# Kernel optimization log

Measured on AMD Instinct MI355X. Metric: run time of the kernel, lower is better.

## Reference

```python
import jax, jax.numpy as jnp
import numpy as np

N_NODES, N_EDGES, IN_F = 20000, 320000, 64
H1, H2 = 2, 2          # attn heads per GATv2 layer
D1, D2 = 128, 128      # gnn_size per layer
NM = [128, 128]        # nodemlp hidden sizes
EM = [512, 256]        # edgemlp hidden sizes
OUT_F = 1
NEG_SLOPE = 0.2


def _lin_init(key, fan_in, fan_out):
    kw, kb = jax.random.split(key)
    s = 1.0 / np.sqrt(fan_in)
    return (jax.random.uniform(kw, (fan_in, fan_out), jnp.float32, -s, s),
            jax.random.uniform(kb, (fan_out,), jnp.float32, -s, s))


def setup_inputs() -> dict:
    key = jax.random.key(0)
    ks = jax.random.split(key, 16)
    x = jax.random.normal(ks[0], (N_NODES, IN_F), jnp.float32)
    src = jax.random.randint(ks[1], (N_EDGES,), 0, N_NODES, jnp.int32)
    dst = jax.random.randint(ks[2], (N_EDGES,), 0, N_NODES, jnp.int32)
    # NodeMLP
    nw0, nb0 = _lin_init(ks[3], IN_F, NM[0])
    nw1, nb1 = _lin_init(ks[4], NM[0], NM[1])
    # GATv2 layer 1 (in=IN_F -> H1*D1)
    g1ws, g1bs = _lin_init(ks[5], IN_F, H1 * D1)
    g1wd, g1bd = _lin_init(ks[6], IN_F, H1 * D1)
    g1a = jax.random.normal(ks[7], (H1, D1), jnp.float32) * (1.0 / np.sqrt(D1))
    # GATv2 layer 2 (in=H1*D1 -> H2*D2)
    g2ws, g2bs = _lin_init(ks[8], H1 * D1, H2 * D2)
    g2wd, g2bd = _lin_init(ks[9], H1 * D1, H2 * D2)
    g2a = jax.random.normal(ks[10], (H2, D2), jnp.float32) * (1.0 / np.sqrt(D2))
    # EdgeMLP: in = 2*(NM[-1] + H2*D2) = 768
    e_in = 2 * (NM[-1] + H2 * D2)
    ew0, eb0 = _lin_init(ks[11], e_in, EM[0])
    ew1, eb1 = _lin_init(ks[12], EM[0], EM[1])
    ew2, eb2 = _lin_init(ks[13], EM[1], OUT_F)
    return dict(x=x, src=src, dst=dst,
                nw0=nw0, nb0=nb0, nw1=nw1, nb1=nb1,
                g1ws=g1ws, g1bs=g1bs, g1wd=g1wd, g1bd=g1bd, g1a=g1a,
                g2ws=g2ws, g2bs=g2bs, g2wd=g2wd, g2bd=g2bd, g2a=g2a,
                ew0=ew0, eb0=eb0, ew1=ew1, eb1=eb1, ew2=ew2, eb2=eb2)


def _segment_softmax(logits, dst, n):
    # logits: (E, H); softmax over edges sharing the same dst node
    m = jax.ops.segment_max(logits, dst, num_segments=n)
    e = jnp.exp(logits - m[dst])
    s = jax.ops.segment_sum(e, dst, num_segments=n)
    return e / s[dst]


def _gatv2(h, src, dst, ws, bs, wd, bd, attn, heads, dim, n):
    fs = (h @ ws + bs).reshape(n, heads, dim)   # fc_src
    fd = (h @ wd + bd).reshape(n, heads, dim)   # fc_dst
    e = jax.nn.leaky_relu(fs[src] + fd[dst], NEG_SLOPE)      # (E,H,D)
    logits = jnp.einsum('ehd,hd->eh', e, attn)               # (E,H)
    a = _segment_softmax(logits, dst, n)                      # (E,H)
    out = jax.ops.segment_sum(a[..., None] * fs[src], dst, num_segments=n)
    return jax.nn.relu(out).reshape(n, heads * dim)           # flatten heads


def reference(x, src, dst,
              nw0, nb0, nw1, nb1,
              g1ws, g1bs, g1wd, g1bd, g1a,
              g2ws, g2bs, g2wd, g2bd, g2a,
              ew0, eb0, ew1, eb1, ew2, eb2):
    n = x.shape[0]
    # NodeMLP (dropout=0 -> identity)
    h1 = jax.nn.relu(x @ nw0 + nb0)
    h1 = jax.nn.relu(h1 @ nw1 + nb1)
    # GCN: two GATv2Conv layers with relu activation, heads flattened
    h2 = _gatv2(x, src, dst, g1ws, g1bs, g1wd, g1bd, g1a, H1, D1, n)
    h2 = _gatv2(h2, src, dst, g2ws, g2bs, g2wd, g2bd, g2a, H2, D2, n)
    # EdgeMLP: gather src/dst, concat, MLP (relu before every layer but first)
    h = jnp.concatenate([h1[src], h1[dst], h2[src], h2[dst]], axis=1)  # (E,768)
    h = h @ ew0 + eb0
    h = jax.nn.relu(h) @ ew1 + eb1
    h = jax.nn.relu(h) @ ew2 + eb2
    return h  # (E, 1) edge scores
```

## Files before the change

### kernel.cpp

```cpp
#include <hip/hip_runtime.h>
#include <hip/hip_bf16.h>

constexpr int N_NODES = 20000;
constexpr int N_EDGES = 320000;

typedef _Float16 half8 __attribute__((ext_vector_type(8)));
typedef _Float16 half4 __attribute__((ext_vector_type(4)));
typedef float    f32x16 __attribute__((ext_vector_type(16)));

__device__ __forceinline__ float lrelu(float x) { return x > 0.f ? x : 0.2f * x; }

__global__ void hist_kernel(const int* __restrict__ dst, int* __restrict__ counts) {
    int e = blockIdx.x * 256 + threadIdx.x;
    if (e < N_EDGES) atomicAdd(&counts[dst[e]], 1);
}

__global__ void scan_all_kernel(const int* __restrict__ counts,
                                int* __restrict__ row_off, int* __restrict__ cursor) {
    __shared__ int ps[1024];
    const int t = threadIdx.x;
    const int base = t * 20;
    int loc[20];
    int sum = 0;
#pragma unroll
    for (int i = 0; i < 20; ++i) {
        const int idx = base + i;
        const int v = (idx < N_NODES) ? counts[idx] : 0;
        loc[i] = sum;
        sum += v;
    }
    ps[t] = sum;
    __syncthreads();
    for (int off = 1; off < 1024; off <<= 1) {
        const int v = (t >= off) ? ps[t - off] : 0;
        __syncthreads();
        ps[t] += v;
        __syncthreads();
    }
    const int ex = ps[t] - sum;
#pragma unroll
    for (int i = 0; i < 20; ++i) {
        const int idx = base + i;
        if (idx < N_NODES) {
            row_off[idx] = ex + loc[i];
            cursor[idx]  = ex + loc[i];
        }
    }
    if (t == 0) row_off[N_NODES] = N_EDGES;
}

__global__ void scatter_kernel(const int* __restrict__ src, const int* __restrict__ dst,
                               int* __restrict__ cursor, int* __restrict__ eidx,
                               int* __restrict__ srcs) {
    int e = blockIdx.x * 256 + threadIdx.x;
    if (e < N_EDGES) {
        int p = atomicAdd(&cursor[dst[e]], 1);
        eidx[p] = e;
        srcs[p] = src[e];
    }
}

template <int K, int M>
__device__ __forceinline__ void pack_one(int idx, const float* __restrict__ W,
                                         int r1, int k1, int r2, int joff, int ldw,
                                         _Float16* __restrict__ H,
                                         _Float16* __restrict__ L) {
    const int l  = idx & 63;
    const int t  = (idx >> 6) % (M / 32);
    const int s  = (idx >> 6) / (M / 32);
    const int j  = joff + t * 32 + (l & 31);
    const int kb = s * 16 + (l >> 5) * 8;
    half8 vh, vl;
#pragma unroll
    for (int i = 0; i < 8; ++i) {
        const int k    = kb + i;
        const int rrow = (k < k1) ? (r1 + k) : (r2 + (k - k1));
        const float w  = W[(size_t)rrow * ldw + j];
        const _Float16 h = (_Float16)w;
        vh[i] = h;
        vl[i] = (_Float16)(w - (float)h);
    }
    reinterpret_cast<half8*>(H)[idx] = vh;
    reinterpret_cast<half8*>(L)[idx] = vl;
}

constexpr int OFF_W1  = 0;
constexpr int OFF_G2S = 16384;
constexpr int OFF_G2D = 24576;
constexpr int OFF_SW0 = 32768;
constexpr int OFF_SW1 = 45056;
constexpr int OFF_DW0 = 57344;
constexpr int OFF_DW1 = 69632;
constexpr int OFF_N1  = 81920;
constexpr int OFF_X   = 83968;
constexpr int PACK_TOT = 89088;

struct PackIn {
    const float *ew1, *g1ws, *g1wd, *g2ws, *g2wd, *ew0, *nw0, *nw1;
    _Float16 *H, *L;
};

__global__ void prepack_all_kernel(PackIn a) {
    const int idx = blockIdx.x * 256 + threadIdx.x;
    if (idx >= PACK_TOT) return;
    _Float16* H = a.H;
    _Float16* L = a.L;
    if (idx < OFF_G2S)
        pack_one<512, 256>(idx - OFF_W1, a.ew1, 0, 512, 0, 0, 256,
                           H + OFF_W1 * 8, L + OFF_W1 * 8);
    else if (idx < OFF_G2D)
        pack_one<256, 256>(idx - OFF_G2S, a.g2ws, 0, 256, 0, 0, 256,
                           H + OFF_G2S * 8, L + OFF_G2S * 8);
    else if (idx < OFF_SW0)
        pack_one<256, 256>(idx - OFF_G2D, a.g2wd, 0, 256, 0, 0, 256,
                           H + OFF_G2D * 8, L + OFF_G2D * 8);
    else if (idx < OFF_SW1)
        pack_one<384, 256>(idx - OFF_SW0, a.ew0, 0, 128, 256, 0, 512,
                           H + OFF_SW0 * 8, L + OFF_SW0 * 8);
    else if (idx < OFF_DW0)
        pack_one<384, 256>(idx - OFF_SW1, a.ew0, 0, 128, 256, 256, 512,
                           H + OFF_SW1 * 8, L + OFF_SW1 * 8);
    else if (idx < OFF_DW1)
        pack_one<384, 256>(idx - OFF_DW0, a.ew0, 128, 128, 512, 0, 512,
                           H + OFF_DW0 * 8, L + OFF_DW0 * 8);
    else if (idx < OFF_N1)
        pack_one<384, 256>(idx - OFF_DW1, a.ew0, 128, 128, 512, 256, 512,
                           H + OFF_DW1 * 8, L + OFF_DW1 * 8);
    else if (idx < OFF_X)
        pack_one<128, 128>(idx - OFF_N1, a.nw1, 0, 128, 0, 0, 128,
                           H + OFF_N1 * 8, L + OFF_N1 * 8);
    else {
        const int xi  = idx - OFF_X;
        const int seg = xi >> 10, r = xi & 1023;
        const int sb  = OFF_X + seg * 1024;
        if (seg == 0)
            pack_one<64, 128>(r, a.nw0, 0, 64, 0, 0, 128, H + sb * 8, L + sb * 8);
        else if (seg <= 2)
            pack_one<64, 128>(r, a.g1ws, 0, 64, 0, (seg - 1) * 128, 256,
                              H + sb * 8, L + sb * 8);
        else
            pack_one<64, 128>(r, a.g1wd, 0, 64, 0, (seg - 3) * 128, 256,
                              H + sb * 8, L + sb * 8);
    }
}

struct LinOut { float* y[6]; const float* b[6]; _Float16* yh[6]; int ldy[6]; int relu[6]; };

template <int K, int TJ, int WR, int K1, int LD1, int LD2, int MINW, int SEG>
__global__ __launch_bounds__(256, MINW) void mfma_linear2_kernel(
    const float* __restrict__ X1, const float* __restrict__ X2,
    const _Float16* __restrict__ BHp, const _Float16* __restrict__ BLp,
    LinOut lo, int N) {
    constexpr int WC    = 4 / WR;
    constexpr int TILES = WC * TJ;
    const int jb  = blockIdx.y;
    const int tid = threadIdx.x;
    const int wv  = tid >> 6, l = tid & 63;
    const int rg  = (WR == 1) ? 0 : ((WR == 4) ? wv : (wv & 1));
    const int cg  = (WR == 1) ? wv : ((WR == 4) ? 0 : (wv >> 1));
    const int m   = l & 31, h = l >> 5;
    const int row = blockIdx.x * (32 * WR) + rg * 32 + m;
    const int ar  = (row < N) ? row : (N - 1);
    const float* __restrict__ xr1 = X1 + (size_t)ar * LD1;
    const float* __restrict__ xr2 = X2 + (size_t)ar * LD2;
    const half8* __restrict__ BH = reinterpret_cast<const half8*>(BHp) + (size_t)jb * SEG;
    const half8* __restrict__ BL = reinterpret_cast<const half8*>(BLp) + (size_t)jb * SEG;
    const float* __restrict__ bp = lo.b[jb];
    float* __restrict__ Y = lo.y[jb];
    _Float16* __restrict__ Yh = lo.yh[jb];
    const int ldy = lo.ldy[jb];
    const int rel = lo.relu[jb];

    f32x16 acc[TJ];
#pragma unroll
    for (int jt = 0; jt < TJ; ++jt) {
        const float bv = bp ? bp[cg * TJ * 32 + jt * 32 + m] : 0.f;
#pragma unroll
        for (int r = 0; r < 16; ++r) acc[jt][r] = bv;
    }

    const int kf = h * 8;
    const float* pf = (kf < K1) ? (xr1 + kf) : (xr2 + (kf - K1));
    float4 xa = *reinterpret_cast<const float4*>(pf);
    float4 xb = *reinterpret_cast<const float4*>(pf + 4);

    for (int s = 0; s < K / 16; ++s) {
        const float xs[8] = {xa.x, xa.y, xa.z, xa.w, xb.x, xb.y, xb.z, xb.w};
        if (s + 1 < K / 16) {
            const int kn = (s + 1) * 16 + h * 8;
            const float* pn = (kn < K1) ? (xr1 + kn) : (xr2 + (kn - K1));
            xa = *reinterpret_cast<const float4*>(pn);
            xb = *reinterpret_cast<const float4*>(pn + 4);
        }
        half8 ah, al;
#pragma unroll
        for (int i = 0; i < 8; ++i) {
            const _Float16 hi = (_Float16)xs[i];
            ah[i] = hi;
            al[i] = (_Float16)(xs[i] - (float)hi);
        }
#pragma unroll
        for (int jt = 0; jt < TJ; ++jt) {
            const int fi = (s * TILES + cg * TJ + jt) * 64 + l;
            const half8 bh = BH[fi];
            const half8 bl = BL[fi];
            acc[jt] = __builtin_amdgcn_mfma_f32_32x32x16_f16(ah, bh, acc[jt], 0, 0, 0);
            acc[jt] = __builtin_amdgcn_mfma_f32_32x32x16_f16(al, bh, acc[jt], 0, 0, 0);
            acc[jt] = __builtin_amdgcn_mfma_f32_32x32x16_f16(ah, bl, acc[jt], 0, 0, 0);
        }
    }

    const int rbase = blockIdx.x * (32 * WR) + rg * 32;
#pragma unroll
    for (int jt = 0; jt < TJ; ++jt) {
        const int j = cg * TJ * 32 + jt * 32 + m;
#pragma unroll
        for (int r = 0; r < 16; ++r) {
            const int orow = rbase + (r & 3) + 8 * (r >> 2) + 4 * h;
            if (orow < N) {
                float v = acc[jt][r];
                if (rel) v = fmaxf(v, 0.f);
                if (Y)  Y[(size_t)orow * ldy + j] = v;
                if (Yh) Yh[(size_t)orow * ldy + j] = (_Float16)v;
            }
        }
    }
}

__global__ void gat_fused_kernel(const _Float16* __restrict__ fsh,
                                 const float* __restrict__ fd,
                                 const float* __restrict__ attn,
                                 const int* __restrict__ row_off,
                                 const int* __restrict__ srcs,
                                 float* __restrict__ outp) {
    const int wv = threadIdx.x >> 6, l = threadIdx.x & 63;
    const int n = blockIdx.x * 4 + wv;
    if (n >= N_NODES) return;
    const int base = (l >> 5) * 128 + (l & 31) * 4;
    const float4 fdv = *reinterpret_cast<const float4*>(&fd[n * 256 + base]);
    const float4 av  = *reinterpret_cast<const float4*>(&attn[base]);
    const int s0 = row_off[n], s1 = row_off[n + 1];

    auto LD = [&](int k) {
        return *reinterpret_cast<const half4*>(&fsh[(size_t)srcs[k] * 256 + base]);
    };
    auto LOGIT = [&](const float4& v) {
        float p = lrelu(v.x + fdv.x) * av.x;
        p = fmaf(lrelu(v.y + fdv.y), av.y, p);
        p = fmaf(lrelu(v.z + fdv.z), av.z, p);
        p = fmaf(lrelu(v.w + fdv.w), av.w, p);
        return p;
    };

    float m = -INFINITY, lsum = 0.f;
    float4 acc = {0.f, 0.f, 0.f, 0.f};
    half4 c0 = {0, 0, 0, 0}, c1 = {0, 0, 0, 0}, n0 = {0, 0, 0, 0}, n1 = {0, 0, 0, 0};
    int i = s0;
    if (i     < s1) c0 = LD(i);
    if (i + 1 < s1) c1 = LD(i + 1);
    if (i + 2 < s1) n0 = LD(i + 2);
    if (i + 3 < s1) n1 = LD(i + 3);
    for (; i + 1 < s1; i += 2) {
        const float4 v0 = {(float)c0.x, (float)c0.y, (float)c0.z, (float)c0.w};
        const float4 v1 = {(float)c1.x, (float)c1.y, (float)c1.z, (float)c1.w};
        c0 = n0; c1 = n1;
        if (i + 4 < s1) n0 = LD(i + 4);
        if (i + 5 < s1) n1 = LD(i + 5);
        float p0 = LOGIT(v0);
        float p1 = LOGIT(v1);
#pragma unroll
        for (int off = 1; off < 32; off <<= 1) {
            p0 += __shfl_xor(p0, off);
            p1 += __shfl_xor(p1, off);
        }
        const float mn = fmaxf(m, fmaxf(p0, p1));
        const float alpha = __expf(m - mn);
        const float w0 = __expf(p0 - mn), w1 = __expf(p1 - mn);
        lsum = fmaf(lsum, alpha, w0 + w1);
        acc.x = fmaf(w1, v1.x, fmaf(w0, v0.x, acc.x * alpha));
        acc.y = fmaf(w1, v1.y, fmaf(w0, v0.y, acc.y * alpha));
        acc.z = fmaf(w1, v1.z, fmaf(w0, v0.z, acc.z * alpha));
        acc.w = fmaf(w1, v1.w, fmaf(w0, v0.w, acc.w * alpha));
        m = mn;
    }
    if (i < s1) {
        const float4 v0 = {(float)c0.x, (float)c0.y, (float)c0.z, (float)c0.w};
        float p0 = LOGIT(v0);
#pragma unroll
        for (int off = 1; off < 32; off <<= 1) p0 += __shfl_xor(p0, off);
        const float mn = fmaxf(m, p0);
        const float alpha = __expf(m - mn);
        const float w0 = __expf(p0 - mn);
        lsum = fmaf(lsum, alpha, w0);
        acc.x = fmaf(w0, v0.x, acc.x * alpha);
        acc.y = fmaf(w0, v0.y, acc.y * alpha);
        acc.z = fmaf(w0, v0.z, acc.z * alpha);
        acc.w = fmaf(w0, v0.w, acc.w * alpha);
    }
    const float inv = (s1 > s0) ? 1.f / lsum : 0.f;
    float4 o;
    o.x = fmaxf(acc.x * inv, 0.f);
    o.y = fmaxf(acc.y * inv, 0.f);
    o.z = fmaxf(acc.z * inv, 0.f);
    o.w = fmaxf(acc.w * inv, 0.f);
    *reinterpret_cast<float4*>(&outp[n * 256 + base]) = o;
}

__global__ __launch_bounds__(256, 2) void edge_mlp8_kernel(
    const _Float16* __restrict__ S, const _Float16* __restrict__ Dn,
    const int* __restrict__ srcs, const int* __restrict__ eidx,
    const int* __restrict__ dstf,
    const _Float16* __restrict__ WpH,
    const float* __restrict__ b1, const float* __restrict__ w2,
    const float* __restrict__ b2, float* __restrict__ out) {
    const int tid = threadIdx.x;
    const int wv  = tid >> 6, l = tid & 63;
    const int m   = l & 31, h = l >> 5;
    const int e0  = blockIdx.x * 128;
    const int slot = e0 + wv * 32 + m;
    const _Float16* __restrict__ Srow = S  + (size_t)srcs[slot] * 512;
    const _Float16* __restrict__ Drow = Dn + (size_t)dstf[eidx[slot]] * 512;
    const half8* __restrict__ Bp = reinterpret_cast<const half8*>(WpH);

    f32x16 acc[8];
#pragma unroll
    for (int jt = 0; jt < 8; ++jt) {
        const float bv = b1[jt * 32 + m];
#pragma unroll
        for (int r = 0; r < 16; ++r) acc[jt][r] = bv;
    }

    half8 bA[8], bB[8];
#pragma unroll
    for (int jt = 0; jt < 8; ++jt) bA[jt] = Bp[jt * 64 + l];
    half8 sv = *reinterpret_cast<const half8*>(Srow + h * 8);
    half8 dv = *reinterpret_cast<const half8*>(Drow + h * 8);

    for (int s = 0; s < 32; s += 2) {
        half8 xh;
#pragma unroll
        for (int i = 0; i < 8; ++i) {
            const _Float16 t = sv[i] + dv[i];
            xh[i] = t > (_Float16)0.f ? t : (_Float16)0.f;
        }
        {
            const int ko = (s + 1) * 16 + h * 8;
            sv = *reinterpret_cast<const half8*>(Srow + ko);
            dv = *reinterpret_cast<const half8*>(Drow + ko);
        }
#pragma unroll
        for (int jt = 0; jt < 8; ++jt)
            bB[jt] = Bp[(size_t)((s + 1) * 8 + jt) * 64 + l];
#pragma unroll
        for (int jt = 0; jt < 8; ++jt)
            acc[jt] = __builtin_amdgcn_mfma_f32_32x32x16_f16(xh, bA[jt], acc[jt], 0, 0, 0);

        half8 xh2;
#pragma unroll
        for (int i = 0; i < 8; ++i) {
            const _Float16 t = sv[i] + dv[i];
            xh2[i] = t > (_Float16)0.f ? t : (_Float16)0.f;
        }
        if (s + 2 < 32) {
            const int ko = (s + 2) * 16 + h * 8;
            sv = *reinterpret_cast<const half8*>(Srow + ko);
            dv = *reinterpret_cast<const half8*>(Drow + ko);
#pragma unroll
            for (int jt = 0; jt < 8; ++jt)
                bA[jt] = Bp[(size_t)((s + 2) * 8 + jt) * 64 + l];
        }
#pragma unroll
        for (int jt = 0; jt < 8; ++jt)
            acc[jt] = __builtin_amdgcn_mfma_f32_32x32x16_f16(xh2, bB[jt], acc[jt], 0, 0, 0);
    }

    float part[16];
#pragma unroll
    for (int r = 0; r < 16; ++r) part[r] = 0.f;
#pragma unroll
    for (int jt = 0; jt < 8; ++jt) {
        const float w2v = w2[jt * 32 + m];
#pragma unroll
        for (int r = 0; r < 16; ++r)
            part[r] = fmaf(fmaxf(acc[jt][r], 0.f), w2v, part[r]);
    }
#pragma unroll
    for (int off = 1; off < 32; off <<= 1)
#pragma unroll
        for (int r = 0; r < 16; ++r) part[r] += __shfl_xor(part[r], off);
    if (m == 0) {
        const float b2v = b2[0];
#pragma unroll
        for (int r = 0; r < 16; ++r) {
            const int row = (r & 3) + 8 * (r >> 2) + 4 * h;
            out[eidx[e0 + wv * 32 + row]] = part[r] + b2v;
        }
    }
}

extern "C" void kernel_launch(void* const* d_in, const int* in_sizes, int n_in,
                              void* d_out, int out_size, void* d_ws, size_t ws_size,
                              hipStream_t stream) {
    (void)in_sizes; (void)n_in; (void)out_size; (void)ws_size;
    const float* x    = (const float*)d_in[0];
    const int*   src  = (const int*)d_in[1];
    const int*   dst  = (const int*)d_in[2];
    const float* nw0  = (const float*)d_in[3];
    const float* nb0  = (const float*)d_in[4];
    const float* nw1  = (const float*)d_in[5];
    const float* nb1  = (const float*)d_in[6];
    const float* g1ws = (const float*)d_in[7];
    const float* g1bs = (const float*)d_in[8];
    const float* g1wd = (const float*)d_in[9];
    const float* g1bd = (const float*)d_in[10];
    const float* g1a  = (const float*)d_in[11];
    const float* g2ws = (const float*)d_in[12];
    const float* g2bs = (const float*)d_in[13];
    const float* g2wd = (const float*)d_in[14];
    const float* g2bd = (const float*)d_in[15];
    const float* g2a  = (const float*)d_in[16];
    const float* ew0  = (const float*)d_in[17];
    const float* eb0  = (const float*)d_in[18];
    const float* ew1  = (const float*)d_in[19];
    const float* eb1  = (const float*)d_in[20];
    const float* ew2  = (const float*)d_in[21];
    const float* eb2  = (const float*)d_in[22];
    float* out = (float*)d_out;

    float* wsF = (float*)d_ws;
    float* h1  = wsF;
    float* g2o = wsF + 2560000;
    float* fsb = wsF + 7680000;
    float* fdb = wsF + 12800000;
    float* g1o = wsF + 17920000;
    _Float16* Sh = (_Float16*)(wsF + 7680000);
    _Float16* Dh = (_Float16*)(wsF + 12800000);
    _Float16* fsh = (_Float16*)(wsF + 23040000);
    int* wsI     = (int*)(wsF + 28160000);
    int* row_off = wsI;
    int* cursor  = wsI + 20016;
    int* eidx    = wsI + 40032;
    int* srcs    = wsI + 360032;
    _Float16* pkH = (_Float16*)((char*)d_ws + 115361280);
    _Float16* pkL = pkH + (size_t)PACK_TOT * 8;

    hipMemsetAsync(cursor, 0, N_NODES * sizeof(int), stream);
    hist_kernel<<<1250, 256, 0, stream>>>(dst, cursor);
    scan_all_kernel<<<1, 1024, 0, stream>>>(cursor, row_off, cursor);
    scatter_kernel<<<1250, 256, 0, stream>>>(src, dst, cursor, eidx, srcs);

    PackIn pin{ew1, g1ws, g1wd, g2ws, g2wd, ew0, nw0, nw1, pkH, pkL};
    prepack_all_kernel<<<(PACK_TOT + 255) / 256, 256, 0, stream>>>(pin);

    {   LinOut lo{};
        lo.y[0] = fsb;        lo.b[0] = nb0;        lo.ldy[0] = 128; lo.relu[0] = 1;
        lo.yh[1] = fsh;       lo.b[1] = g1bs;       lo.ldy[1] = 256;
        lo.yh[2] = fsh + 128; lo.b[2] = g1bs + 128; lo.ldy[2] = 256;
        lo.y[3] = fdb;        lo.b[3] = g1bd;       lo.ldy[3] = 256;
        lo.y[4] = fdb + 128;  lo.b[4] = g1bd + 128; lo.ldy[4] = 256;
        mfma_linear2_kernel<64, 1, 1, 64, 64, 64, 4, 1024>
            <<<dim3(625, 5), 256, 0, stream>>>(x, x, pkH + OFF_X * 8, pkL + OFF_X * 8,
                                               lo, N_NODES); }

    {   LinOut lo{};
        lo.y[0] = h1; lo.b[0] = nb1; lo.ldy[0] = 128; lo.relu[0] = 1;
        mfma_linear2_kernel<128, 1, 1, 128, 128, 128, 4, 0>
            <<<dim3(625, 1), 256, 0, stream>>>(fsb, fsb, pkH + OFF_N1 * 8, pkL + OFF_N1 * 8,
                                               lo, N_NODES); }

    gat_fused_kernel<<<5000, 256, 0, stream>>>(fsh, fdb, g1a, row_off, srcs, g1o);

    {   LinOut lo{};
        lo.yh[0] = fsh; lo.b[0] = g2bs; lo.ldy[0] = 256;
        lo.y[1] = fdb;  lo.b[1] = g2bd; lo.ldy[1] = 256;
        mfma_linear2_kernel<256, 8, 4, 256, 256, 256, 2, 8192>
            <<<dim3(157, 2), 256, 0, stream>>>(g1o, g1o, pkH + OFF_G2S * 8, pkL + OFF_G2S * 8,
                                               lo, N_NODES); }
    gat_fused_kernel<<<5000, 256, 0, stream>>>(fsh, fdb, g2a, row_off, srcs, g2o);

    {   LinOut lo{};
        lo.yh[0] = Sh;       lo.ldy[0] = 512;
        lo.yh[1] = Sh + 256; lo.ldy[1] = 512;
        lo.yh[2] = Dh;       lo.b[2] = eb0;       lo.ldy[2] = 512;
        lo.yh[3] = Dh + 256; lo.b[3] = eb0 + 256; lo.ldy[3] = 512;
        mfma_linear2_kernel<384, 8, 4, 128, 128, 256, 2, 12288>
            <<<dim3(157, 4), 256, 0, stream>>>(h1, g2o, pkH + OFF_SW0 * 8, pkL + OFF_SW0 * 8,
                                               lo, N_NODES); }

    edge_mlp8_kernel<<<N_EDGES / 128, 256, 0, stream>>>(Sh, Dh, srcs, eidx, dst,
                                                        pkH + OFF_W1 * 8,
                                                        eb1, ew2, eb2, out);
}
```

Before: 571.3 us.

## Stage edge-MLP weights in shared memory and drop softmax max tracking

The edge MLP kernel now loads each weight slice once per block and double-buffers it in LDS, with a block barrier every k-step. Previously every wave fetched the full weight slice from global memory into registers. This trades redundant global/L2 traffic and register pressure for 32 __syncthreads and LDS reads. The GAT aggregation also drops the online-softmax running max and rescaling, exponentiating raw logits directly. That removes per-edge exp and multiply work but risks overflow if logits are large.

Result: faster. 536.1 us (-6.2%).

```diff
diff --git a/kernel.cpp b/kernel.cpp
--- a/kernel.cpp
+++ b/kernel.cpp
@@ -252,7 +252,7 @@
         return p;
     };
 
-    float m = -INFINITY, lsum = 0.f;
+    float lsum = 0.f;
     float4 acc = {0.f, 0.f, 0.f, 0.f};
     half4 c0 = {0, 0, 0, 0}, c1 = {0, 0, 0, 0}, n0 = {0, 0, 0, 0}, n1 = {0, 0, 0, 0};
     int i = s0;
@@ -273,29 +273,24 @@
             p0 += __shfl_xor(p0, off);
             p1 += __shfl_xor(p1, off);
         }
-        const float mn = fmaxf(m, fmaxf(p0, p1));
-        const float alpha = __expf(m - mn);
-        const float w0 = __expf(p0 - mn), w1 = __expf(p1 - mn);
-        lsum = fmaf(lsum, alpha, w0 + w1);
-        acc.x = fmaf(w1, v1.x, fmaf(w0, v0.x, acc.x * alpha));
-        acc.y = fmaf(w1, v1.y, fmaf(w0, v0.y, acc.y * alpha));
-        acc.z = fmaf(w1, v1.z, fmaf(w0, v0.z, acc.z * alpha));
-        acc.w = fmaf(w1, v1.w, fmaf(w0, v0.w, acc.w * alpha));
-        m = mn;
+        const float w0 = __expf(p0), w1 = __expf(p1);
+        lsum += w0 + w1;
+        acc.x = fmaf(w1, v1.x, fmaf(w0, v0.x, acc.x));
+        acc.y = fmaf(w1, v1.y, fmaf(w0, v0.y, acc.y));
+        acc.z = fmaf(w1, v1.z, fmaf(w0, v0.z, acc.z));
+        acc.w = fmaf(w1, v1.w, fmaf(w0, v0.w, acc.w));
     }
     if (i < s1) {
         const float4 v0 = {(float)c0.x, (float)c0.y, (float)c0.z, (float)c0.w};
         float p0 = LOGIT(v0);
 #pragma unroll
         for (int off = 1; off < 32; off <<= 1) p0 += __shfl_xor(p0, off);
-        const float mn = fmaxf(m, p0);
-        const float alpha = __expf(m - mn);
-        const float w0 = __expf(p0 - mn);
-        lsum = fmaf(lsum, alpha, w0);
-        acc.x = fmaf(w0, v0.x, acc.x * alpha);
-        acc.y = fmaf(w0, v0.y, acc.y * alpha);
-        acc.z = fmaf(w0, v0.z, acc.z * alpha);
-        acc.w = fmaf(w0, v0.w, acc.w * alpha);
+        const float w0 = __expf(p0);
+        lsum += w0;
+        acc.x = fmaf(w0, v0.x, acc.x);
+        acc.y = fmaf(w0, v0.y, acc.y);
+        acc.z = fmaf(w0, v0.z, acc.z);
+        acc.w = fmaf(w0, v0.w, acc.w);
     }
     const float inv = (s1 > s0) ? 1.f / lsum : 0.f;
     float4 o;
@@ -306,13 +301,14 @@
     *reinterpret_cast<float4*>(&outp[n * 256 + base]) = o;
 }
 
-__global__ __launch_bounds__(256, 2) void edge_mlp8_kernel(
+__global__ __launch_bounds__(256, 2) void edge_mlp7_kernel(
     const _Float16* __restrict__ S, const _Float16* __restrict__ Dn,
     const int* __restrict__ srcs, const int* __restrict__ eidx,
     const int* __restrict__ dstf,
     const _Float16* __restrict__ WpH,
     const float* __restrict__ b1, const float* __restrict__ w2,
     const float* __restrict__ b2, float* __restrict__ out) {
+    __shared__ __align__(16) _Float16 Bs[2][8][512];
     const int tid = threadIdx.x;
     const int wv  = tid >> 6, l = tid & 63;
     const int m   = l & 31, h = l >> 5;
@@ -320,7 +316,6 @@
     const int slot = e0 + wv * 32 + m;
     const _Float16* __restrict__ Srow = S  + (size_t)srcs[slot] * 512;
     const _Float16* __restrict__ Drow = Dn + (size_t)dstf[eidx[slot]] * 512;
-    const half8* __restrict__ Bp = reinterpret_cast<const half8*>(WpH);
 
     f32x16 acc[8];
 #pragma unroll
@@ -330,48 +325,51 @@
         for (int r = 0; r < 16; ++r) acc[jt][r] = bv;
     }
 
-    half8 bA[8], bB[8];
-#pragma unroll
-    for (int jt = 0; jt < 8; ++jt) bA[jt] = Bp[jt * 64 + l];
+#pragma unroll
+    for (int c = 0; c < 2; ++c) {
+        const int jt = wv * 2 + c;
+        *reinterpret_cast<float4*>(&Bs[0][jt][l * 8]) =
+            *reinterpret_cast<const float4*>(WpH + ((size_t)jt * 64 + l) * 8);
+    }
     half8 sv = *reinterpret_cast<const half8*>(Srow + h * 8);
     half8 dv = *reinterpret_cast<const half8*>(Drow + h * 8);
-
-    for (int s = 0; s < 32; s += 2) {
+    __syncthreads();
+
+    for (int s = 0; s < 32; ++s) {
+        const int buf = s & 1;
+        float4 bst[2];
+        if (s < 31) {
+#pragma unroll
+            for (int c = 0; c < 2; ++c) {
+                const int jt = wv * 2 + c;
+                bst[c] = *reinterpret_cast<const float4*>(
+                    WpH + ((size_t)((s + 1) * 8 + jt) * 64 + l) * 8);
+            }
+        }
         half8 xh;
 #pragma unroll
         for (int i = 0; i < 8; ++i) {
             const _Float16 t = sv[i] + dv[i];
             xh[i] = t > (_Float16)0.f ? t : (_Float16)0.f;
         }
-        {
+        if (s < 31) {
             const int ko = (s + 1) * 16 + h * 8;
             sv = *reinterpret_cast<const half8*>(Srow + ko);
             dv = *reinterpret_cast<const half8*>(Drow + ko);
         }
 #pragma unroll
-        for (int jt = 0; jt < 8; ++jt)
-            bB[jt] = Bp[(size_t)((s + 1) * 8 + jt) * 64 + l];
-#pragma unroll
-        for (int jt = 0; jt < 8; ++jt)
-            acc[jt] = __builtin_amdgcn_mfma_f32_32x32x16_f16(xh, bA[jt], acc[jt], 0, 0, 0);
-
-        half8 xh2;
-#pragma unroll
-        for (int i = 0; i < 8; ++i) {
-            const _Float16 t = sv[i] + dv[i];
-            xh2[i] = t > (_Float16)0.f ? t : (_Float16)0.f;
-        }
-        if (s + 2 < 32) {
-            const int ko = (s + 2) * 16 + h * 8;
-            sv = *reinterpret_cast<const half8*>(Srow + ko);
-            dv = *reinterpret_cast<const half8*>(Drow + ko);
-#pragma unroll
-            for (int jt = 0; jt < 8; ++jt)
-                bA[jt] = Bp[(size_t)((s + 2) * 8 + jt) * 64 + l];
-        }
-#pragma unroll
-        for (int jt = 0; jt < 8; ++jt)
-            acc[jt] = __builtin_amdgcn_mfma_f32_32x32x16_f16(xh2, bB[jt], acc[jt], 0, 0, 0);
+        for (int jt = 0; jt < 8; ++jt) {
+            const half8 bh = *reinterpret_cast<const half8*>(&Bs[buf][jt][l * 8]);
+            acc[jt] = __builtin_amdgcn_mfma_f32_32x32x16_f16(xh, bh, acc[jt], 0, 0, 0);
+        }
+        if (s < 31) {
+#pragma unroll
+            for (int c = 0; c < 2; ++c) {
+                const int jt = wv * 2 + c;
+                *reinterpret_cast<float4*>(&Bs[buf ^ 1][jt][l * 8]) = bst[c];
+            }
+        }
+        __syncthreads();
     }
 
     float part[16];
@@ -487,7 +485,7 @@
             <<<dim3(157, 4), 256, 0, stream>>>(h1, g2o, pkH + OFF_SW0 * 8, pkL + OFF_SW0 * 8,
                                                lo, N_NODES); }
 
-    edge_mlp8_kernel<<<N_EDGES / 128, 256, 0, stream>>>(Sh, Dh, srcs, eidx, dst,
+    edge_mlp7_kernel<<<N_EDGES / 128, 256, 0, stream>>>(Sh, Dh, srcs, eidx, dst,
                                                         pkH + OFF_W1 * 8,
                                                         eb1, ew2, eb2, out);
 }
```
